# Performance work log

Measured on AMD Instinct MI355X. Metric: run time of the kernel, lower is better.

The kernel has to match this reference:

```python
import jax, jax.numpy as jnp
import numpy as np

B, S, E, H, FF = 2, 2048, 768, 12, 3072
D = E // H
EPS = 1e-5


def setup_inputs() -> dict:
    key = jax.random.key(0)
    ks = jax.random.split(key, 12)
    sc = lambda n: 1.0 / np.sqrt(n)
    return {
        "x": jax.random.normal(ks[0], (B, S, E), jnp.float32),
        "wq": jax.random.normal(ks[1], (E, E), jnp.float32) * sc(E),
        "wk": jax.random.normal(ks[2], (E, E), jnp.float32) * sc(E),
        "wv": jax.random.normal(ks[3], (E, E), jnp.float32) * sc(E),
        "wo": jax.random.normal(ks[4], (E, E), jnp.float32) * sc(E),
        "bo": jax.random.normal(ks[5], (E,), jnp.float32) * 0.02,
        "w1": jax.random.normal(ks[6], (FF, E), jnp.float32) * sc(E),
        "b1": jax.random.normal(ks[7], (FF,), jnp.float32) * 0.02,
        "w2": jax.random.normal(ks[8], (E, FF), jnp.float32) * sc(FF),
        "b2": jax.random.normal(ks[9], (E,), jnp.float32) * 0.02,
        "gamma": jnp.ones((E,), jnp.float32),
        "beta": jnp.zeros((E,), jnp.float32),
    }


def _layernorm(x, g, b):
    mu = jnp.mean(x, axis=-1, keepdims=True)
    var = jnp.mean(jnp.square(x - mu), axis=-1, keepdims=True)
    return (x - mu) * jax.lax.rsqrt(var + EPS) * g + b


def reference(x, wq, wk, wv, wo, bo, w1, b1, w2, b2, gamma, beta):
    res = x
    xn = _layernorm(x, gamma, beta)
    # Q/K/V projections (torch Linear: y = x @ W.T), split into heads
    q = (xn @ wq.T).reshape(B, S, H, D)
    k = (xn @ wk.T).reshape(B, S, H, D)
    v = (xn @ wv.T).reshape(B, S, H, D)
    scale = jnp.sqrt(jnp.float32(D))
    scores = jnp.einsum("bqhd,bkhd->bhqk", q, k) / scale  # [B,H,S,S]
    causal = jnp.tril(jnp.ones((S, S), bool))
    scores = jnp.where(causal, scores, -jnp.inf)
    w = jax.nn.softmax(scores, axis=-1)
    attn = jnp.einsum("bhqk,bkhd->bqhd", w, v).reshape(B, S, E)
    attn = attn @ wo.T + bo
    res = res + attn
    y = _layernorm(res, gamma, beta)  # NOTE: same LayerNorm params reused (as in source)
    h = jax.nn.gelu(y @ w1.T + b1, approximate=False)  # nn.GELU default is exact erf
    ffn = h @ w2.T + b2
    return res + ffn
```

## Files before the change

kernel.cpp:

```cpp
#include <hip/hip_runtime.h>
#include <hip/hip_bf16.h>
#include <math.h>

typedef __bf16 bf16_8 __attribute__((ext_vector_type(8)));
typedef float f32x4 __attribute__((ext_vector_type(4)));

__global__ __launch_bounds__(256) void ln_kernel(
    const float* __restrict__ x, const float* __restrict__ g,
    const float* __restrict__ b, __hip_bfloat16* __restrict__ out, int cols) {
  const int row = blockIdx.x;
  const int t = threadIdx.x;
  float loc[3];
  float s = 0.f, s2 = 0.f;
#pragma unroll
  for (int i = 0; i < 3; ++i) {
    float v = x[(size_t)row * cols + t + i * 256];
    loc[i] = v;
    s += v;
    s2 += v * v;
  }
#pragma unroll
  for (int off = 32; off; off >>= 1) {
    s += __shfl_down(s, off);
    s2 += __shfl_down(s2, off);
  }
  __shared__ float red[2][4];
  const int lane = t & 63, w = t >> 6;
  if (lane == 0) {
    red[0][w] = s;
    red[1][w] = s2;
  }
  __syncthreads();
  s = red[0][0] + red[0][1] + red[0][2] + red[0][3];
  s2 = red[1][0] + red[1][1] + red[1][2] + red[1][3];
  const float mu = s / cols;
  const float var = s2 / cols - mu * mu;
  const float rs = rsqrtf(var + 1e-5f);
  __hip_bfloat16* orow = out + (size_t)row * cols;
#pragma unroll
  for (int i = 0; i < 3; ++i) {
    int c = t + i * 256;
    orow[c] = __hip_bfloat16((loc[i] - mu) * rs * g[c] + b[c]);
  }
}

template <int MODE>
__global__ __launch_bounds__(256) void gemm_bt(
    const __hip_bfloat16* __restrict__ A, const float* __restrict__ B0,
    const float* __restrict__ B1, const float* __restrict__ B2,
    const float* __restrict__ bias, void* __restrict__ out,
    int M, int N, int K) {
  constexpr int BM = 128, BN = 128, BK = 32, LDP = 40;
  __shared__ __align__(16) __bf16 As[BM * LDP];
  __shared__ __align__(16) __bf16 Bs[BN * LDP];
  const int tid = threadIdx.x;
  const int m0 = blockIdx.y * BM;
  const int n0 = blockIdx.x * BN;
  const int wave = tid >> 6;
  const int lane = tid & 63;
  const int quad = lane >> 4;
  const int l16 = lane & 15;
  const int wm = (wave & 1) * 64;
  const int wn = (wave >> 1) * 64;

  int tsel = 0, nloc = n0;
  const float* Bw = B0;
  if constexpr (MODE == 0) {
    tsel = n0 / 768;
    nloc = n0 - tsel * 768;
    Bw = (tsel == 0) ? B0 : (tsel == 1) ? B1 : B2;
  }
  int kbase = 0, kcnt = K;
  if constexpr (MODE == 2) {
    kcnt = K / gridDim.z;
    kbase = blockIdx.z * kcnt;
  }

  f32x4 acc[4][4] = {};

  for (int k0 = kbase; k0 < kbase + kcnt; k0 += BK) {
    __syncthreads();
#pragma unroll
    for (int u = 0; u < 2; ++u) {
      int i = tid + u * 256;
      int row = i >> 2, kq = i & 3;
      *(bf16_8*)(&As[row * LDP + kq * 8]) =
          *(const bf16_8*)(A + (size_t)(m0 + row) * K + k0 + kq * 8);
      const float* src = Bw + (size_t)(nloc + row) * K + k0 + kq * 8;
      float4 f0 = *(const float4*)src;
      float4 f1 = *(const float4*)(src + 4);
      bf16_8 bv;
      bv[0] = (__bf16)f0.x; bv[1] = (__bf16)f0.y; bv[2] = (__bf16)f0.z; bv[3] = (__bf16)f0.w;
      bv[4] = (__bf16)f1.x; bv[5] = (__bf16)f1.y; bv[6] = (__bf16)f1.z; bv[7] = (__bf16)f1.w;
      *(bf16_8*)(&Bs[row * LDP + kq * 8]) = bv;
    }
    __syncthreads();
    bf16_8 af[4], bfr[4];
#pragma unroll
    for (int i = 0; i < 4; ++i)
      af[i] = *(const bf16_8*)(&As[(wm + i * 16 + l16) * LDP + quad * 8]);
#pragma unroll
    for (int j = 0; j < 4; ++j)
      bfr[j] = *(const bf16_8*)(&Bs[(wn + j * 16 + l16) * LDP + quad * 8]);
#pragma unroll
    for (int i = 0; i < 4; ++i)
#pragma unroll
      for (int j = 0; j < 4; ++j)
        acc[i][j] =
            __builtin_amdgcn_mfma_f32_16x16x32_bf16(af[i], bfr[j], acc[i][j], 0, 0, 0);
  }

#pragma unroll
  for (int i = 0; i < 4; ++i) {
#pragma unroll
    for (int j = 0; j < 4; ++j) {
#pragma unroll
      for (int r = 0; r < 4; ++r) {
        const int row = m0 + wm + i * 16 + quad * 4 + r;
        const int coll = nloc + wn + j * 16 + l16;
        const float v = acc[i][j][r];
        if constexpr (MODE == 0) {
          const size_t idx = (size_t)tsel * M * 768 + (size_t)row * 768 + coll;
          ((__hip_bfloat16*)out)[idx] = __hip_bfloat16(v);
        } else if constexpr (MODE == 1) {
          const size_t idx = (size_t)row * N + coll;
          float tt = v + bias[coll];
          float gl = 0.5f * tt * (1.0f + erff(tt * 0.70710678118654752f));
          ((__hip_bfloat16*)out)[idx] = __hip_bfloat16(gl);
        } else {
          const size_t idx = (size_t)row * N + coll;
          float add = v + (blockIdx.z == 0 ? bias[coll] : 0.f);
          atomicAdd((float*)out + idx, add);
        }
      }
    }
  }
}

__global__ void zero_ctr(int* __restrict__ c) {
  if (threadIdx.x == 0) *c = 0;
}

#define ALDP 72
__global__ __launch_bounds__(256) void attn_mfma(
    const __hip_bfloat16* __restrict__ qb, const __hip_bfloat16* __restrict__ kb,
    const __hip_bfloat16* __restrict__ vb, __hip_bfloat16* __restrict__ ob,
    int* __restrict__ ctr) {
  const int S = 2048, H = 12, E = 768;
  const int tid = threadIdx.x;
  const int wave = tid >> 6;
  const int lane = tid & 63;
  const int quad = lane >> 4;
  const int l16 = lane & 15;

  __shared__ __align__(16) __bf16 Ks[64 * ALDP];
  __shared__ __align__(16) __bf16 Vt[64 * ALDP];
  __shared__ __align__(16) __bf16 Pl[4][16 * ALDP];
  __shared__ int task;

  for (;;) {
    if (tid == 0) task = atomicAdd(ctr, 1);
    __syncthreads();
    const int t = task;
    if (t >= 24 * 32) return;
    const int qblk = 31 - (t / 24);
    const int bh = t - (t / 24) * 24;
    const int b = bh / H, h = bh - b * H;
    const int q0 = qblk * 64;
    const int qw = q0 + wave * 16;
    const size_t base = (size_t)b * S * E + (size_t)h * 64;

    bf16_8 qf[2];
#pragma unroll
    for (int s = 0; s < 2; ++s)
      qf[s] = *(const bf16_8*)(qb + base + (size_t)(qw + l16) * E + s * 32 + quad * 8);

    f32x4 o[4] = {};
    float mq = -1e30f, lq = 0.f;

    for (int kt = 0; kt <= qblk; ++kt) {
      const int k0 = kt * 64;
      __syncthreads();
#pragma unroll
      for (int u = 0; u < 2; ++u) {
        int i = tid + u * 256;
        int kr = i >> 3, kc = i & 7;
        *(bf16_8*)(&Ks[kr * ALDP + kc * 8]) =
            *(const bf16_8*)(kb + base + (size_t)(k0 + kr) * E + kc * 8);
      }
#pragma unroll
      for (int u = 0; u < 2; ++u) {
        int i = tid + u * 256;
        int kr = i & 63, dq = i >> 6;
        bf16_8 vv = *(const bf16_8*)(vb + base + (size_t)(k0 + kr) * E + dq * 8);
#pragma unroll
        for (int j = 0; j < 8; ++j) Vt[(dq * 8 + j) * ALDP + kr] = vv[j];
      }
      __syncthreads();

      f32x4 sc[4] = {};
#pragma unroll
      for (int jj = 0; jj < 4; ++jj)
#pragma unroll
        for (int s = 0; s < 2; ++s) {
          bf16_8 kf = *(const bf16_8*)(&Ks[(jj * 16 + l16) * ALDP + s * 32 + quad * 8]);
          sc[jj] = __builtin_amdgcn_mfma_f32_16x16x32_bf16(kf, qf[s], sc[jj], 0, 0, 0);
        }

      float mx = -1e30f;
#pragma unroll
      for (int jj = 0; jj < 4; ++jj)
#pragma unroll
        for (int r = 0; r < 4; ++r) {
          float v = sc[jj][r] * 0.125f;
          if (kt == qblk && (k0 + jj * 16 + quad * 4 + r) > (qw + l16)) v = -1e30f;
          sc[jj][r] = v;
          mx = fmaxf(mx, v);
        }
      mx = fmaxf(mx, __shfl_xor(mx, 16));
      mx = fmaxf(mx, __shfl_xor(mx, 32));
      const float mn = fmaxf(mq, mx);
      const float corr = __expf(mq - mn);
      mq = mn;
      float sum = 0.f;
#pragma unroll
      for (int jj = 0; jj < 4; ++jj)
#pragma unroll
        for (int r = 0; r < 4; ++r) {
          float p = __expf(sc[jj][r] - mn);
          sc[jj][r] = p;
          sum += p;
        }
      sum += __shfl_xor(sum, 16);
      sum += __shfl_xor(sum, 32);
      lq = lq * corr + sum;
#pragma unroll
      for (int nt = 0; nt < 4; ++nt)
#pragma unroll
        for (int r = 0; r < 4; ++r) o[nt][r] *= corr;

      __bf16* pw = &Pl[wave][0];
#pragma unroll
      for (int jj = 0; jj < 4; ++jj)
#pragma unroll
        for (int r = 0; r < 4; ++r)
          pw[l16 * ALDP + jj * 16 + quad * 4 + r] = (__bf16)sc[jj][r];

#pragma unroll
      for (int s = 0; s < 2; ++s) {
        bf16_8 pf = *(const bf16_8*)(&pw[l16 * ALDP + s * 32 + quad * 8]);
#pragma unroll
        for (int dt = 0; dt < 4; ++dt) {
          bf16_8 vf = *(const bf16_8*)(&Vt[(dt * 16 + l16) * ALDP + s * 32 + quad * 8]);
          o[dt] = __builtin_amdgcn_mfma_f32_16x16x32_bf16(vf, pf, o[dt], 0, 0, 0);
        }
      }
    }

    const float inv = 1.f / lq;
    __bf16* pw = &Pl[wave][0];
#pragma unroll
    for (int dt = 0; dt < 4; ++dt)
#pragma unroll
      for (int r = 0; r < 4; ++r)
        pw[l16 * ALDP + dt * 16 + quad * 4 + r] = (__bf16)(o[dt][r] * inv);
#pragma unroll
    for (int u = 0; u < 2; ++u) {
      int j = lane + u * 64;
      int ql = j >> 3, ch = j & 7;
      bf16_8 ov = *(const bf16_8*)(&pw[ql * ALDP + ch * 8]);
      *(bf16_8*)(ob + base + (size_t)(qw + ql) * E + ch * 8) = ov;
    }
  }
}

extern "C" void kernel_launch(void* const* d_in, const int* in_sizes, int n_in,
                              void* d_out, int out_size, void* d_ws, size_t ws_size,
                              hipStream_t stream) {
  const int Bv = 2, S = 2048, E = 768, FF = 3072;
  const int M = Bv * S;

  const float* x = (const float*)d_in[0];
  const float* wq = (const float*)d_in[1];
  const float* wk = (const float*)d_in[2];
  const float* wv = (const float*)d_in[3];
  const float* wo = (const float*)d_in[4];
  const float* bo = (const float*)d_in[5];
  const float* w1 = (const float*)d_in[6];
  const float* b1 = (const float*)d_in[7];
  const float* w2 = (const float*)d_in[8];
  const float* b2 = (const float*)d_in[9];
  const float* gamma = (const float*)d_in[10];
  const float* beta = (const float*)d_in[11];

  int* ctr = (int*)d_ws;
  __hip_bfloat16* slot = (__hip_bfloat16*)((char*)d_ws + 256);
  const size_t ME = (size_t)M * E;
  __hip_bfloat16* xn = slot;
  __hip_bfloat16* attn = slot;
  __hip_bfloat16* y = slot;
  __hip_bfloat16* q = slot + ME;
  __hip_bfloat16* k = slot + 2 * ME;
  __hip_bfloat16* v = slot + 3 * ME;
  __hip_bfloat16* hbuf = slot + ME;
  float* res = (float*)d_out;

  ln_kernel<<<M, 256, 0, stream>>>(x, gamma, beta, xn, E);
  gemm_bt<0><<<dim3(18, 32), 256, 0, stream>>>(xn, wq, wk, wv, nullptr, q, M, 2304, E);
  zero_ctr<<<1, 64, 0, stream>>>(ctr);
  attn_mfma<<<768, 256, 0, stream>>>(q, k, v, attn, ctr);
  hipMemcpyAsync(d_out, x, ME * sizeof(float), hipMemcpyDeviceToDevice, stream);
  gemm_bt<2><<<dim3(6, 32, 2), 256, 0, stream>>>(attn, wo, nullptr, nullptr, bo, res, M, E, E);
  ln_kernel<<<M, 256, 0, stream>>>(res, gamma, beta, y, E);
  gemm_bt<1><<<dim3(24, 32), 256, 0, stream>>>(y, w1, nullptr, nullptr, b1, hbuf, M, FF, E);
  gemm_bt<2><<<dim3(6, 32, 4), 256, 0, stream>>>(hbuf, w2, nullptr, nullptr, b2, d_out, M, E, FF);
}
```

Measured before the change: 358.2 us.

## Pre-convert weights to bf16 and use direct global-to-LDS loads in GEMM

```diff
diff --git a/kernel.cpp b/kernel.cpp
--- a/kernel.cpp
+++ b/kernel.cpp
@@ -3,6 +3,7 @@
 #include <math.h>
 
 typedef __bf16 bf16_8 __attribute__((ext_vector_type(8)));
+typedef __bf16 bf16_4 __attribute__((ext_vector_type(4)));
 typedef float f32x4 __attribute__((ext_vector_type(4)));
 
 __global__ __launch_bounds__(256) void ln_kernel(
@@ -44,15 +45,32 @@
   }
 }
 
+__global__ __launch_bounds__(256) void cvt_multi(
+    const float* __restrict__ sa, const float* __restrict__ sb,
+    const float* __restrict__ sc, const float* __restrict__ sd,
+    __hip_bfloat16* __restrict__ da, __hip_bfloat16* __restrict__ db,
+    __hip_bfloat16* __restrict__ dc, __hip_bfloat16* __restrict__ dd) {
+  const float* src;
+  __hip_bfloat16* dst;
+  if (blockIdx.y == 0) { src = sa; dst = da; }
+  else if (blockIdx.y == 1) { src = sb; dst = db; }
+  else if (blockIdx.y == 2) { src = sc; dst = dc; }
+  else { src = sd; dst = dd; }
+  const size_t i = ((size_t)blockIdx.x * 256 + threadIdx.x) * 4;
+  float4 f = *(const float4*)(src + i);
+  bf16_4 o;
+  o[0] = (__bf16)f.x; o[1] = (__bf16)f.y; o[2] = (__bf16)f.z; o[3] = (__bf16)f.w;
+  *(bf16_4*)((__bf16*)dst + i) = o;
+}
+
 template <int MODE>
 __global__ __launch_bounds__(256) void gemm_bt(
-    const __hip_bfloat16* __restrict__ A, const float* __restrict__ B0,
-    const float* __restrict__ B1, const float* __restrict__ B2,
+    const __hip_bfloat16* __restrict__ A, const __hip_bfloat16* __restrict__ B,
     const float* __restrict__ bias, void* __restrict__ out,
-    int M, int N, int K) {
-  constexpr int BM = 128, BN = 128, BK = 32, LDP = 40;
-  __shared__ __align__(16) __bf16 As[BM * LDP];
-  __shared__ __align__(16) __bf16 Bs[BN * LDP];
+    int M, int N, int K, int lda, int ldb, int ldout) {
+  constexpr int BM = 128, BN = 128, BK = 64;
+  __shared__ __align__(16) __bf16 As[BM * BK];
+  __shared__ __align__(16) __bf16 Bs[BN * BK];
   const int tid = threadIdx.x;
   const int m0 = blockIdx.y * BM;
   const int n0 = blockIdx.x * BN;
@@ -63,51 +81,47 @@
   const int wm = (wave & 1) * 64;
   const int wn = (wave >> 1) * 64;
 
-  int tsel = 0, nloc = n0;
-  const float* Bw = B0;
-  if constexpr (MODE == 0) {
-    tsel = n0 / 768;
-    nloc = n0 - tsel * 768;
-    Bw = (tsel == 0) ? B0 : (tsel == 1) ? B1 : B2;
-  }
   int kbase = 0, kcnt = K;
   if constexpr (MODE == 2) {
     kcnt = K / gridDim.z;
     kbase = blockIdx.z * kcnt;
   }
 
+  const int srow = lane >> 3;
+  const int scol = (lane & 7) * 8;
+  const __hip_bfloat16* Ap = A + (size_t)(m0 + wave * 8 + srow) * lda + kbase + scol;
+  const __hip_bfloat16* Bp = B + (size_t)(n0 + wave * 8 + srow) * ldb + kbase + scol;
+
   f32x4 acc[4][4] = {};
 
-  for (int k0 = kbase; k0 < kbase + kcnt; k0 += BK) {
+  for (int k0 = 0; k0 < kcnt; k0 += BK) {
     __syncthreads();
 #pragma unroll
-    for (int u = 0; u < 2; ++u) {
-      int i = tid + u * 256;
-      int row = i >> 2, kq = i & 3;
-      *(bf16_8*)(&As[row * LDP + kq * 8]) =
-          *(const bf16_8*)(A + (size_t)(m0 + row) * K + k0 + kq * 8);
-      const float* src = Bw + (size_t)(nloc + row) * K + k0 + kq * 8;
-      float4 f0 = *(const float4*)src;
-      float4 f1 = *(const float4*)(src + 4);
-      bf16_8 bv;
-      bv[0] = (__bf16)f0.x; bv[1] = (__bf16)f0.y; bv[2] = (__bf16)f0.z; bv[3] = (__bf16)f0.w;
-      bv[4] = (__bf16)f1.x; bv[5] = (__bf16)f1.y; bv[6] = (__bf16)f1.z; bv[7] = (__bf16)f1.w;
-      *(bf16_8*)(&Bs[row * LDP + kq * 8]) = bv;
+    for (int u = 0; u < 4; ++u) {
+      __builtin_amdgcn_global_load_lds(
+          (const __attribute__((address_space(1))) void*)(Ap + (size_t)(u * 32) * lda + k0),
+          (__attribute__((address_space(3))) void*)(&As[(u * 32 + wave * 8) * BK]), 16, 0, 0);
+      __builtin_amdgcn_global_load_lds(
+          (const __attribute__((address_space(1))) void*)(Bp + (size_t)(u * 32) * ldb + k0),
+          (__attribute__((address_space(3))) void*)(&Bs[(u * 32 + wave * 8) * BK]), 16, 0, 0);
     }
     __syncthreads();
-    bf16_8 af[4], bfr[4];
-#pragma unroll
-    for (int i = 0; i < 4; ++i)
-      af[i] = *(const bf16_8*)(&As[(wm + i * 16 + l16) * LDP + quad * 8]);
-#pragma unroll
-    for (int j = 0; j < 4; ++j)
-      bfr[j] = *(const bf16_8*)(&Bs[(wn + j * 16 + l16) * LDP + quad * 8]);
-#pragma unroll
-    for (int i = 0; i < 4; ++i)
+#pragma unroll
+    for (int kk = 0; kk < 2; ++kk) {
+      bf16_8 af[4], bfr[4];
+#pragma unroll
+      for (int i = 0; i < 4; ++i)
+        af[i] = *(const bf16_8*)(&As[(wm + i * 16 + l16) * BK + kk * 32 + quad * 8]);
 #pragma unroll
       for (int j = 0; j < 4; ++j)
-        acc[i][j] =
-            __builtin_amdgcn_mfma_f32_16x16x32_bf16(af[i], bfr[j], acc[i][j], 0, 0, 0);
+        bfr[j] = *(const bf16_8*)(&Bs[(wn + j * 16 + l16) * BK + kk * 32 + quad * 8]);
+#pragma unroll
+      for (int i = 0; i < 4; ++i)
+#pragma unroll
+        for (int j = 0; j < 4; ++j)
+          acc[i][j] =
+              __builtin_amdgcn_mfma_f32_16x16x32_bf16(af[i], bfr[j], acc[i][j], 0, 0, 0);
+    }
   }
 
 #pragma unroll
@@ -117,20 +131,19 @@
 #pragma unroll
       for (int r = 0; r < 4; ++r) {
         const int row = m0 + wm + i * 16 + quad * 4 + r;
-        const int coll = nloc + wn + j * 16 + l16;
+        const int col = n0 + wn + j * 16 + l16;
         const float v = acc[i][j][r];
         if constexpr (MODE == 0) {
-          const size_t idx = (size_t)tsel * M * 768 + (size_t)row * 768 + coll;
+          const int tsel = n0 / 768;
+          const size_t idx = ((size_t)tsel * M + row) * 768 + (col - tsel * 768);
           ((__hip_bfloat16*)out)[idx] = __hip_bfloat16(v);
         } else if constexpr (MODE == 1) {
-          const size_t idx = (size_t)row * N + coll;
-          float tt = v + bias[coll];
+          float tt = v + bias[col];
           float gl = 0.5f * tt * (1.0f + erff(tt * 0.70710678118654752f));
-          ((__hip_bfloat16*)out)[idx] = __hip_bfloat16(gl);
+          ((__hip_bfloat16*)out)[(size_t)row * ldout + col] = __hip_bfloat16(gl);
         } else {
-          const size_t idx = (size_t)row * N + coll;
-          float add = v + (blockIdx.z == 0 ? bias[coll] : 0.f);
-          atomicAdd((float*)out + idx, add);
+          float add = v + ((blockIdx.z == 0 && bias) ? bias[col] : 0.f);
+          atomicAdd((float*)out + (size_t)row * 768 + col, add);
         }
       }
     }
@@ -279,6 +292,9 @@
                               hipStream_t stream) {
   const int Bv = 2, S = 2048, E = 768, FF = 3072;
   const int M = Bv * S;
+  const size_t ME = (size_t)M * E;
+  const size_t EE = (size_t)E * E;
+  const size_t EF = (size_t)E * FF;
 
   const float* x = (const float*)d_in[0];
   const float* wq = (const float*)d_in[1];
@@ -295,23 +311,28 @@
 
   int* ctr = (int*)d_ws;
   __hip_bfloat16* slot = (__hip_bfloat16*)((char*)d_ws + 256);
-  const size_t ME = (size_t)M * E;
-  __hip_bfloat16* xn = slot;
-  __hip_bfloat16* attn = slot;
-  __hip_bfloat16* y = slot;
-  __hip_bfloat16* q = slot + ME;
-  __hip_bfloat16* k = slot + 2 * ME;
-  __hip_bfloat16* v = slot + 3 * ME;
-  __hip_bfloat16* hbuf = slot + ME;
+  __hip_bfloat16* s0 = slot;
+  __hip_bfloat16* s1 = slot + ME;
+  __hip_bfloat16* s2 = slot + 2 * ME;
+  __hip_bfloat16* s3 = slot + 3 * ME;
+  __hip_bfloat16* s4 = slot + 4 * ME;
   float* res = (float*)d_out;
 
-  ln_kernel<<<M, 256, 0, stream>>>(x, gamma, beta, xn, E);
-  gemm_bt<0><<<dim3(18, 32), 256, 0, stream>>>(xn, wq, wk, wv, nullptr, q, M, 2304, E);
+  cvt_multi<<<dim3(EE / 1024, 4), 256, 0, stream>>>(
+      wq, wk, wv, wo, s4, s4 + EE, s4 + 2 * EE, s4 + 3 * EE);
+  ln_kernel<<<M, 256, 0, stream>>>(x, gamma, beta, s0, E);
+  gemm_bt<0><<<dim3(18, 32), 256, 0, stream>>>(s0, s4, nullptr, s1, M, 2304, E, E, E, 0);
   zero_ctr<<<1, 64, 0, stream>>>(ctr);
-  attn_mfma<<<768, 256, 0, stream>>>(q, k, v, attn, ctr);
+  attn_mfma<<<768, 256, 0, stream>>>(s1, s2, s3, s0, ctr);
   hipMemcpyAsync(d_out, x, ME * sizeof(float), hipMemcpyDeviceToDevice, stream);
-  gemm_bt<2><<<dim3(6, 32, 2), 256, 0, stream>>>(attn, wo, nullptr, nullptr, bo, res, M, E, E);
-  ln_kernel<<<M, 256, 0, stream>>>(res, gamma, beta, y, E);
-  gemm_bt<1><<<dim3(24, 32), 256, 0, stream>>>(y, w1, nullptr, nullptr, b1, hbuf, M, FF, E);
-  gemm_bt<2><<<dim3(6, 32, 4), 256, 0, stream>>>(hbuf, w2, nullptr, nullptr, b2, d_out, M, E, FF);
-}
+  gemm_bt<2><<<dim3(6, 32, 2), 256, 0, stream>>>(s0, s4 + 3 * EE, bo, res, M, E, E, E, E, 0);
+  cvt_multi<<<dim3(EF / 1024, 2), 256, 0, stream>>>(
+      w1, w2, nullptr, nullptr, s3, s4, nullptr, nullptr);
+  ln_kernel<<<M, 256, 0, stream>>>(res, gamma, beta, s0, E);
+  gemm_bt<1><<<dim3(12, 32), 256, 0, stream>>>(s0, s3, b1, s1, M, 1536, E, E, E, 1536);
+  gemm_bt<2><<<dim3(6, 32, 2), 256, 0, stream>>>(s1, s4, b2, res, M, E, 1536, 1536, FF, 0);
+  gemm_bt<1><<<dim3(12, 32), 256, 0, stream>>>(
+      s0, s3 + (size_t)1536 * E, b1 + 1536, s1, M, 1536, E, E, E, 1536);
+  gemm_bt<2><<<dim3(6, 32, 2), 256, 0, stream>>>(
+      s1, s4 + 1536, nullptr, res, M, E, 1536, 1536, FF, 0);
+}
```

New measurement: 406.1 us. 13.4% more time.
